# Performance work log

Hardware: AMD Instinct MI355X
Metric: run time of the kernel (lower is better)

The kernel has to match this reference:

```python
import jax, jax.numpy as jnp
import numpy as np

B, S, D, E, K = 4, 4096, 2048, 64, 2

def setup_inputs() -> dict:
    key = jax.random.key(0)
    kx, kw = jax.random.split(key)
    x = jax.random.normal(kx, (B, S, D), dtype=jnp.float32)
    W = jax.random.normal(kw, (E, D), dtype=jnp.float32) * (1.0 / np.sqrt(D))
    b = jnp.zeros((E,), dtype=jnp.float32)
    return {"x": x, "W": W, "b": b, "k": K}

def reference(x, W, b, k):
    # logits: [B, S, E]
    logits = jnp.einsum('bsd,ed->bse', x, W) + b
    probs = jax.nn.softmax(logits, axis=-1)
    topk_probs, topk_experts = jax.lax.top_k(probs, k)  # [B,S,k]
    # one-hot over experts, OR-reduce over k -> bool mask [B,S,E]
    onehot = jax.nn.one_hot(topk_experts, E, dtype=jnp.int32)  # [B,S,k,E]
    masks = onehot.sum(axis=-2).astype(jnp.bool_)
    return (masks, probs)
```

## Files before the change

### kernel.cpp

```cpp
#include <hip/hip_runtime.h>
#include <math.h>

#define NTOK    16384
#define DDIM    2048
#define NEXP    64
#define PSTRIDE (NTOK * NEXP)
#define ITERS   32
#define SLICE_B 8192

#define AS1 __attribute__((address_space(1)))
#define AS3 __attribute__((address_space(3)))

typedef _Float16 half8   __attribute__((ext_vector_type(8)));
typedef float    floatx4 __attribute__((ext_vector_type(4)));

__global__ __launch_bounds__(256) void wconv_kernel(
    const float* __restrict__ W, _Float16* __restrict__ ws)
{
    const int g     = blockIdx.x * 256 + threadIdx.x;
    const int i32   = g >> 9;
    const int L     = g & 511;
    const int plane = L >> 8;
    const int r     = L & 255;
    const int e     = r >> 2;
    const int cp    = r & 3;
    const int c     = cp ^ ((e >> 1) & 3);
    const int k     = (i32 << 5) + (c << 3);

    const float* src = &W[(size_t)e * DDIM + k];
    floatx4 w0 = *(const floatx4*)src;
    floatx4 w1 = *(const floatx4*)(src + 4);

    half8 o;
#pragma unroll
    for (int i = 0; i < 4; ++i) {
        float f0 = w0[i], f1 = w1[i];
        _Float16 h0 = (_Float16)f0, h1 = (_Float16)f1;
        if (plane == 0) { o[i] = h0; o[4 + i] = h1; }
        else {
            o[i]     = (_Float16)((f0 - (float)h0) * 2048.0f);
            o[4 + i] = (_Float16)((f1 - (float)h1) * 2048.0f);
        }
    }
    *(half8*)((char*)ws + (size_t)g * 16) = o;
}

__global__ __launch_bounds__(256, 2) void router_kernel(
    const float* __restrict__ x,
    const _Float16* __restrict__ ws,
    const float* __restrict__ bias,
    float* __restrict__ out)
{
    __shared__ __align__(16) char wlds[4][2][SLICE_B];

    const int tid  = threadIdx.x;
    const int lane = tid & 63;
    const int wid  = tid >> 6;
    const int t    = wid >> 1;
    const int h    = wid & 1;
    const int t0   = blockIdx.x * 32 + t * 16;
    const int mrow = lane & 15;
    const int quad = lane >> 4;

    floatx4 acc_hh[4], acc_md[4];
#pragma unroll
    for (int j = 0; j < 4; ++j) { acc_hh[j] = (floatx4)0.0f; acc_md[j] = (floatx4)0.0f; }

    const float* xrow = x + (size_t)(t0 + mrow) * DDIM + h * 1024 + quad * 8;
    const char* wsrc = (const char*)ws + (size_t)h * 32 * SLICE_B + lane * 16;
    char* buf0 = &wlds[wid][0][0];
    char* buf1 = &wlds[wid][1][0];

    int boff[4];
#pragma unroll
    for (int j = 0; j < 4; ++j) {
        const int e = j * 16 + mrow;
        boff[j] = e * 32 + ((quad ^ ((e >> 1) & 3)) << 3);
    }

#define DMA_SLICE(I, DST)                                                      \
    {                                                                          \
        const char* gs = wsrc + (size_t)(I) * SLICE_B;                         \
        _Pragma("unroll")                                                      \
        for (int q = 0; q < 8; ++q)                                            \
            __builtin_amdgcn_global_load_lds(                                  \
                (const AS1 unsigned int*)(const void*)(gs + q * 1024),         \
                (AS3 unsigned int*)(void*)((DST) + q * 1024), 16, 0, 0);       \
    }

    DMA_SLICE(0, buf0);
    floatx4 xa0 = *(const floatx4*)(xrow);
    floatx4 xa1 = *(const floatx4*)(xrow + 4);
    floatx4 xb0 = *(const floatx4*)(xrow + 32);
    floatx4 xb1 = *(const floatx4*)(xrow + 36);

#pragma unroll 2
    for (int i = 0; i < ITERS; ++i) {
        if (i + 1 < ITERS) DMA_SLICE(i + 1, (i & 1) ? buf0 : buf1);
        floatx4 xn0, xn1;
        if (i + 2 < ITERS) {
            xn0 = *(const floatx4*)(xrow + (i + 2) * 32);
            xn1 = *(const floatx4*)(xrow + (i + 2) * 32 + 4);
        }

        half8 a_hi, a_lo;
#pragma unroll
        for (int q = 0; q < 4; ++q) {
            float fv = xa0[q];
            _Float16 hh = (_Float16)fv;
            a_hi[q] = hh;
            a_lo[q] = (_Float16)((fv - (float)hh) * 2048.0f);
        }
#pragma unroll
        for (int q = 0; q < 4; ++q) {
            float fv = xa1[q];
            _Float16 hh = (_Float16)fv;
            a_hi[4 + q] = hh;
            a_lo[4 + q] = (_Float16)((fv - (float)hh) * 2048.0f);
        }

        const _Float16* lb = (const _Float16*)((i & 1) ? buf1 : buf0);
#pragma unroll
        for (int j = 0; j < 4; ++j) {
            half8 bh = *(const half8*)(lb + boff[j]);
            half8 bl = *(const half8*)(lb + 2048 + boff[j]);
            acc_hh[j] = __builtin_amdgcn_mfma_f32_16x16x32_f16(a_hi, bh, acc_hh[j], 0, 0, 0);
            acc_md[j] = __builtin_amdgcn_mfma_f32_16x16x32_f16(a_hi, bl, acc_md[j], 0, 0, 0);
            acc_md[j] = __builtin_amdgcn_mfma_f32_16x16x32_f16(a_lo, bh, acc_md[j], 0, 0, 0);
        }

        xa0 = xb0; xa1 = xb1; xb0 = xn0; xb1 = xn1;
    }

    float lg[4][4];
#pragma unroll
    for (int j = 0; j < 4; ++j)
#pragma unroll
        for (int r = 0; r < 4; ++r)
            lg[j][r] = acc_hh[j][r] + acc_md[j][r] * (1.0f / 2048.0f);

    __syncthreads();
    float* rbuf = (float*)&wlds[0][0][0];
    if (h == 1) {
#pragma unroll
        for (int j = 0; j < 4; ++j)
#pragma unroll
            for (int r = 0; r < 4; ++r)
                rbuf[t * 1024 + (j * 4 + r) * 64 + lane] = lg[j][r];
    }
    __syncthreads();
    if (h == 1) return;

#pragma unroll
    for (int j = 0; j < 4; ++j) {
        const float bj = bias[j * 16 + mrow];
#pragma unroll
        for (int r = 0; r < 4; ++r)
            lg[j][r] += rbuf[t * 1024 + (j * 4 + r) * 64 + lane] + bj;
    }

    const int c = mrow;
#pragma unroll
    for (int r = 0; r < 4; ++r) {
        const int trow = t0 + quad * 4 + r;

        float m = lg[0][r];
#pragma unroll
        for (int j = 1; j < 4; ++j) m = fmaxf(m, lg[j][r]);
#pragma unroll
        for (int off = 1; off <= 8; off <<= 1) m = fmaxf(m, __shfl_xor(m, off));

        float pj[4], s = 0.0f;
#pragma unroll
        for (int j = 0; j < 4; ++j) { pj[j] = __expf(lg[j][r] - m); s += pj[j]; }
#pragma unroll
        for (int off = 1; off <= 8; off <<= 1) s += __shfl_xor(s, off);
        const float rinv = 1.0f / s;

        float v1 = -1e30f, v2 = -1e30f; int i1 = -1, i2 = -1;
#pragma unroll
        for (int j = 0; j < 4; ++j) {
            float v = lg[j][r]; int e = j * 16 + c;
            if (v > v1 || (v == v1 && e < i1)) { v2 = v1; i2 = i1; v1 = v; i1 = e; }
            else if (v > v2 || (v == v2 && e < i2)) { v2 = v; i2 = e; }
        }
#pragma unroll
        for (int off = 1; off <= 8; off <<= 1) {
            float u1 = __shfl_xor(v1, off); int q1 = __shfl_xor(i1, off);
            float u2 = __shfl_xor(v2, off); int q2 = __shfl_xor(i2, off);
            if (u1 > v1 || (u1 == v1 && q1 < i1)) {
                if (v1 > u2 || (v1 == u2 && i1 < q2)) { v2 = v1; i2 = i1; }
                else                                   { v2 = u2; i2 = q2; }
                v1 = u1; i1 = q1;
            } else {
                if (u1 > v2 || (u1 == v2 && q1 < i2)) { v2 = u1; i2 = q1; }
            }
        }

#pragma unroll
        for (int j = 0; j < 4; ++j) {
            const int col = j * 16 + c;
            const size_t o = (size_t)trow * NEXP + col;
            out[o]           = (col == i1 || col == i2) ? 1.0f : 0.0f;
            out[PSTRIDE + o] = pj[j] * rinv;
        }
    }
}

extern "C" void kernel_launch(void* const* d_in, const int* in_sizes, int n_in,
                              void* d_out, int out_size, void* d_ws, size_t ws_size,
                              hipStream_t stream) {
    const float* x = (const float*)d_in[0];
    const float* W = (const float*)d_in[1];
    const float* b = (const float*)d_in[2];
    (void)in_sizes; (void)n_in; (void)out_size; (void)ws_size;
    float* out = (float*)d_out;

    _Float16* ws = (_Float16*)d_ws;

    hipLaunchKernelGGL(wconv_kernel, dim3(128), dim3(256), 0, stream, W, ws);
    hipLaunchKernelGGL(router_kernel, dim3(NTOK / 32), dim3(256), 0, stream, x, ws, b, out);
}
```

Measured before the change: 225.8 us.

## Load pre-swizzled weight fragments directly from global into registers, drop LDS staging

Reorders the converted fp16 weight workspace so each lane's MFMA B-fragment is a contiguous 16-byte chunk. The router kernel then reads it straight from global/L2 into registers with a one-iteration prefetch, instead of DMAing slices into LDS and reading them back. This removes the LDS staging and the ds_read traffic and shrinks shared memory to the reduction buffer. In exchange, every wave re-reads the weights from cache, and the fully unrolled loop may raise register pressure under the 2-blocks-per-CU launch bound.

Measured after the change: 248.5 us. +10.0%, slower.

```diff
diff --git a/kernel.cpp b/kernel.cpp
--- a/kernel.cpp
+++ b/kernel.cpp
@@ -6,10 +6,6 @@
 #define NEXP    64
 #define PSTRIDE (NTOK * NEXP)
 #define ITERS   32
-#define SLICE_B 8192
-
-#define AS1 __attribute__((address_space(1)))
-#define AS3 __attribute__((address_space(3)))
 
 typedef _Float16 half8   __attribute__((ext_vector_type(8)));
 typedef float    floatx4 __attribute__((ext_vector_type(4)));
@@ -17,15 +13,14 @@
 __global__ __launch_bounds__(256) void wconv_kernel(
     const float* __restrict__ W, _Float16* __restrict__ ws)
 {
-    const int g     = blockIdx.x * 256 + threadIdx.x;
-    const int i32   = g >> 9;
-    const int L     = g & 511;
-    const int plane = L >> 8;
-    const int r     = L & 255;
-    const int e     = r >> 2;
-    const int cp    = r & 3;
-    const int c     = cp ^ ((e >> 1) & 3);
-    const int k     = (i32 << 5) + (c << 3);
+    const int g    = blockIdx.x * 256 + threadIdx.x;
+    const int lane = g & 63;
+    const int pl   = (g >> 6) & 1;
+    const int j    = (g >> 7) & 3;
+    const int i    = (g >> 9) & 31;
+    const int h    = (g >> 14) & 1;
+    const int e    = j * 16 + (lane & 15);
+    const int k    = h * 1024 + i * 32 + (lane >> 4) * 8;
 
     const float* src = &W[(size_t)e * DDIM + k];
     floatx4 w0 = *(const floatx4*)src;
@@ -33,16 +28,16 @@
 
     half8 o;
 #pragma unroll
-    for (int i = 0; i < 4; ++i) {
-        float f0 = w0[i], f1 = w1[i];
+    for (int q = 0; q < 4; ++q) {
+        float f0 = w0[q], f1 = w1[q];
         _Float16 h0 = (_Float16)f0, h1 = (_Float16)f1;
-        if (plane == 0) { o[i] = h0; o[4 + i] = h1; }
+        if (pl == 0) { o[q] = h0; o[4 + q] = h1; }
         else {
-            o[i]     = (_Float16)((f0 - (float)h0) * 2048.0f);
-            o[4 + i] = (_Float16)((f1 - (float)h1) * 2048.0f);
-        }
-    }
-    *(half8*)((char*)ws + (size_t)g * 16) = o;
+            o[q]     = (_Float16)((f0 - (float)h0) * 2048.0f);
+            o[4 + q] = (_Float16)((f1 - (float)h1) * 2048.0f);
+        }
+    }
+    *(half8*)(ws + (size_t)g * 8) = o;
 }
 
 __global__ __launch_bounds__(256, 2) void router_kernel(
@@ -51,7 +46,7 @@
     const float* __restrict__ bias,
     float* __restrict__ out)
 {
-    __shared__ __align__(16) char wlds[4][2][SLICE_B];
+    __shared__ float rbuf[2048];
 
     const int tid  = threadIdx.x;
     const int lane = tid & 63;
@@ -67,69 +62,59 @@
     for (int j = 0; j < 4; ++j) { acc_hh[j] = (floatx4)0.0f; acc_md[j] = (floatx4)0.0f; }
 
     const float* xrow = x + (size_t)(t0 + mrow) * DDIM + h * 1024 + quad * 8;
-    const char* wsrc = (const char*)ws + (size_t)h * 32 * SLICE_B + lane * 16;
-    char* buf0 = &wlds[wid][0][0];
-    char* buf1 = &wlds[wid][1][0];
-
-    int boff[4];
+    const _Float16* wbase = ws + (size_t)h * 131072 + (size_t)lane * 8;
+
+    floatx4 xs0[ITERS], xs1[ITERS];
+    half8   bsh[ITERS][4], bsl[ITERS][4];
+
+#pragma unroll
+    for (int i = 0; i < 2; ++i) {
+        xs0[i] = *(const floatx4*)(xrow + i * 32);
+        xs1[i] = *(const floatx4*)(xrow + i * 32 + 4);
+    }
 #pragma unroll
     for (int j = 0; j < 4; ++j) {
-        const int e = j * 16 + mrow;
-        boff[j] = e * 32 + ((quad ^ ((e >> 1) & 3)) << 3);
-    }
-
-#define DMA_SLICE(I, DST)                                                      \
-    {                                                                          \
-        const char* gs = wsrc + (size_t)(I) * SLICE_B;                         \
-        _Pragma("unroll")                                                      \
-        for (int q = 0; q < 8; ++q)                                            \
-            __builtin_amdgcn_global_load_lds(                                  \
-                (const AS1 unsigned int*)(const void*)(gs + q * 1024),         \
-                (AS3 unsigned int*)(void*)((DST) + q * 1024), 16, 0, 0);       \
-    }
-
-    DMA_SLICE(0, buf0);
-    floatx4 xa0 = *(const floatx4*)(xrow);
-    floatx4 xa1 = *(const floatx4*)(xrow + 4);
-    floatx4 xb0 = *(const floatx4*)(xrow + 32);
-    floatx4 xb1 = *(const floatx4*)(xrow + 36);
-
-#pragma unroll 2
+        bsh[0][j] = *(const half8*)(wbase + (size_t)(j * 2    ) * 512);
+        bsl[0][j] = *(const half8*)(wbase + (size_t)(j * 2 + 1) * 512);
+    }
+
+#pragma unroll
     for (int i = 0; i < ITERS; ++i) {
-        if (i + 1 < ITERS) DMA_SLICE(i + 1, (i & 1) ? buf0 : buf1);
-        floatx4 xn0, xn1;
         if (i + 2 < ITERS) {
-            xn0 = *(const floatx4*)(xrow + (i + 2) * 32);
-            xn1 = *(const floatx4*)(xrow + (i + 2) * 32 + 4);
+            xs0[i + 2] = *(const floatx4*)(xrow + (i + 2) * 32);
+            xs1[i + 2] = *(const floatx4*)(xrow + (i + 2) * 32 + 4);
+        }
+        if (i + 1 < ITERS) {
+            const _Float16* gb = wbase + (size_t)(i + 1) * 4096;
+#pragma unroll
+            for (int j = 0; j < 4; ++j) {
+                bsh[i + 1][j] = *(const half8*)(gb + (size_t)(j * 2    ) * 512);
+                bsl[i + 1][j] = *(const half8*)(gb + (size_t)(j * 2 + 1) * 512);
+            }
         }
 
         half8 a_hi, a_lo;
 #pragma unroll
         for (int q = 0; q < 4; ++q) {
-            float fv = xa0[q];
+            float fv = xs0[i][q];
             _Float16 hh = (_Float16)fv;
             a_hi[q] = hh;
             a_lo[q] = (_Float16)((fv - (float)hh) * 2048.0f);
         }
 #pragma unroll
         for (int q = 0; q < 4; ++q) {
-            float fv = xa1[q];
+            float fv = xs1[i][q];
             _Float16 hh = (_Float16)fv;
             a_hi[4 + q] = hh;
             a_lo[4 + q] = (_Float16)((fv - (float)hh) * 2048.0f);
         }
 
-        const _Float16* lb = (const _Float16*)((i & 1) ? buf1 : buf0);
 #pragma unroll
         for (int j = 0; j < 4; ++j) {
-            half8 bh = *(const half8*)(lb + boff[j]);
-            half8 bl = *(const half8*)(lb + 2048 + boff[j]);
-            acc_hh[j] = __builtin_amdgcn_mfma_f32_16x16x32_f16(a_hi, bh, acc_hh[j], 0, 0, 0);
-            acc_md[j] = __builtin_amdgcn_mfma_f32_16x16x32_f16(a_hi, bl, acc_md[j], 0, 0, 0);
-            acc_md[j] = __builtin_amdgcn_mfma_f32_16x16x32_f16(a_lo, bh, acc_md[j], 0, 0, 0);
-        }
-
-        xa0 = xb0; xa1 = xb1; xb0 = xn0; xb1 = xn1;
+            acc_hh[j] = __builtin_amdgcn_mfma_f32_16x16x32_f16(a_hi, bsh[i][j], acc_hh[j], 0, 0, 0);
+            acc_md[j] = __builtin_amdgcn_mfma_f32_16x16x32_f16(a_hi, bsl[i][j], acc_md[j], 0, 0, 0);
+            acc_md[j] = __builtin_amdgcn_mfma_f32_16x16x32_f16(a_lo, bsh[i][j], acc_md[j], 0, 0, 0);
+        }
     }
 
     float lg[4][4];
@@ -140,7 +125,6 @@
             lg[j][r] = acc_hh[j][r] + acc_md[j][r] * (1.0f / 2048.0f);
 
     __syncthreads();
-    float* rbuf = (float*)&wlds[0][0][0];
     if (h == 1) {
 #pragma unroll
         for (int j = 0; j < 4; ++j)
```

## Share weight LDS slices across waves with 4-way K split per block

Applied to the files above, without the earlier changes.

Each block now runs 512 threads (8 waves: 2 token tiles × 4 K-quarters), and a single double-buffered 32KB LDS slice per phase is loaded cooperatively and shared by all waves. Before, each wave staged its own private weight copy. The weight workspace layout and swizzle are changed to match, and partial logits from three K-quarters are reduced through LDS. This cuts redundant LDS weight traffic per block and raises the wave count. In exchange it adds a block-wide __syncthreads on every phase and a larger cross-wave reduction.

After: 204.6 us. 1.1x faster.

```diff
diff --git a/kernel.cpp b/kernel.cpp
--- a/kernel.cpp
+++ b/kernel.cpp
@@ -5,8 +5,8 @@
 #define DDIM    2048
 #define NEXP    64
 #define PSTRIDE (NTOK * NEXP)
-#define ITERS   32
-#define SLICE_B 8192
+#define NPH     16
+#define SLICE_B 32768
 
 #define AS1 __attribute__((address_space(1)))
 #define AS3 __attribute__((address_space(3)))
@@ -17,15 +17,15 @@
 __global__ __launch_bounds__(256) void wconv_kernel(
     const float* __restrict__ W, _Float16* __restrict__ ws)
 {
-    const int g     = blockIdx.x * 256 + threadIdx.x;
-    const int i32   = g >> 9;
-    const int L     = g & 511;
-    const int plane = L >> 8;
-    const int r     = L & 255;
-    const int e     = r >> 2;
-    const int cp    = r & 3;
-    const int c     = cp ^ ((e >> 1) & 3);
-    const int k     = (i32 << 5) + (c << 3);
+    const int g  = blockIdx.x * 256 + threadIdx.x;
+    const int p  = g >> 11;
+    const int L  = g & 2047;
+    const int qp = L & 3;
+    const int e  = (L >> 2) & 63;
+    const int pl = (L >> 8) & 1;
+    const int h  = (L >> 9) & 3;
+    const int q  = qp ^ ((e ^ (e >> 2)) & 3);
+    const int k  = h * 512 + p * 32 + q * 8;
 
     const float* src = &W[(size_t)e * DDIM + k];
     floatx4 w0 = *(const floatx4*)src;
@@ -36,28 +36,28 @@
     for (int i = 0; i < 4; ++i) {
         float f0 = w0[i], f1 = w1[i];
         _Float16 h0 = (_Float16)f0, h1 = (_Float16)f1;
-        if (plane == 0) { o[i] = h0; o[4 + i] = h1; }
+        if (pl == 0) { o[i] = h0; o[4 + i] = h1; }
         else {
             o[i]     = (_Float16)((f0 - (float)h0) * 2048.0f);
             o[4 + i] = (_Float16)((f1 - (float)h1) * 2048.0f);
         }
     }
-    *(half8*)((char*)ws + (size_t)g * 16) = o;
+    *(half8*)(ws + (size_t)g * 8) = o;
 }
 
-__global__ __launch_bounds__(256, 2) void router_kernel(
+__global__ __launch_bounds__(512, 4) void router_kernel(
     const float* __restrict__ x,
     const _Float16* __restrict__ ws,
     const float* __restrict__ bias,
     float* __restrict__ out)
 {
-    __shared__ __align__(16) char wlds[4][2][SLICE_B];
+    __shared__ __align__(16) char lds[2][SLICE_B];
 
     const int tid  = threadIdx.x;
     const int lane = tid & 63;
     const int wid  = tid >> 6;
-    const int t    = wid >> 1;
-    const int h    = wid & 1;
+    const int t    = wid >> 2;
+    const int h    = wid & 3;
     const int t0   = blockIdx.x * 32 + t * 16;
     const int mrow = lane & 15;
     const int quad = lane >> 4;
@@ -66,70 +66,69 @@
 #pragma unroll
     for (int j = 0; j < 4; ++j) { acc_hh[j] = (floatx4)0.0f; acc_md[j] = (floatx4)0.0f; }
 
-    const float* xrow = x + (size_t)(t0 + mrow) * DDIM + h * 1024 + quad * 8;
-    const char* wsrc = (const char*)ws + (size_t)h * 32 * SLICE_B + lane * 16;
-    char* buf0 = &wlds[wid][0][0];
-    char* buf1 = &wlds[wid][1][0];
+    const float* xrow = x + (size_t)(t0 + mrow) * DDIM + h * 512 + quad * 8;
 
     int boff[4];
 #pragma unroll
     for (int j = 0; j < 4; ++j) {
         const int e = j * 16 + mrow;
-        boff[j] = e * 32 + ((quad ^ ((e >> 1) & 3)) << 3);
-    }
-
-#define DMA_SLICE(I, DST)                                                      \
+        const int s = (e ^ (e >> 2)) & 3;
+        boff[j] = (((h * 2) * 64 + e) * 4 + (quad ^ s)) * 8;
+    }
+
+#define DMA(P, B)                                                              \
     {                                                                          \
-        const char* gs = wsrc + (size_t)(I) * SLICE_B;                         \
+        const char* gs = (const char*)ws + (size_t)(P) * SLICE_B + (size_t)tid * 16; \
+        char*       ld = &lds[B][0] + tid * 16;                                \
         _Pragma("unroll")                                                      \
-        for (int q = 0; q < 8; ++q)                                            \
+        for (int i_ = 0; i_ < 4; ++i_)                                         \
             __builtin_amdgcn_global_load_lds(                                  \
-                (const AS1 unsigned int*)(const void*)(gs + q * 1024),         \
-                (AS3 unsigned int*)(void*)((DST) + q * 1024), 16, 0, 0);       \
-    }
-
-    DMA_SLICE(0, buf0);
-    floatx4 xa0 = *(const floatx4*)(xrow);
-    floatx4 xa1 = *(const floatx4*)(xrow + 4);
-    floatx4 xb0 = *(const floatx4*)(xrow + 32);
-    floatx4 xb1 = *(const floatx4*)(xrow + 36);
+                (const AS1 unsigned int*)(const void*)(gs + i_ * 8192),        \
+                (AS3 unsigned int*)(void*)(ld + i_ * 8192), 16, 0, 0);         \
+    }
+
+    DMA(0, 0);
+    floatx4 xc0 = *(const floatx4*)(xrow);
+    floatx4 xc1 = *(const floatx4*)(xrow + 4);
+    __syncthreads();
 
 #pragma unroll 2
-    for (int i = 0; i < ITERS; ++i) {
-        if (i + 1 < ITERS) DMA_SLICE(i + 1, (i & 1) ? buf0 : buf1);
+    for (int p = 0; p < NPH; ++p) {
         floatx4 xn0, xn1;
-        if (i + 2 < ITERS) {
-            xn0 = *(const floatx4*)(xrow + (i + 2) * 32);
-            xn1 = *(const floatx4*)(xrow + (i + 2) * 32 + 4);
+        if (p < NPH - 1) {
+            DMA(p + 1, (p + 1) & 1);
+            xn0 = *(const floatx4*)(xrow + (p + 1) * 32);
+            xn1 = *(const floatx4*)(xrow + (p + 1) * 32 + 4);
         }
 
         half8 a_hi, a_lo;
 #pragma unroll
         for (int q = 0; q < 4; ++q) {
-            float fv = xa0[q];
+            float fv = xc0[q];
             _Float16 hh = (_Float16)fv;
             a_hi[q] = hh;
             a_lo[q] = (_Float16)((fv - (float)hh) * 2048.0f);
         }
 #pragma unroll
         for (int q = 0; q < 4; ++q) {
-            float fv = xa1[q];
+            float fv = xc1[q];
             _Float16 hh = (_Float16)fv;
             a_hi[4 + q] = hh;
             a_lo[4 + q] = (_Float16)((fv - (float)hh) * 2048.0f);
         }
 
-        const _Float16* lb = (const _Float16*)((i & 1) ? buf1 : buf0);
+        const _Float16* lb = (const _Float16*)lds[p & 1];
 #pragma unroll
         for (int j = 0; j < 4; ++j) {
             half8 bh = *(const half8*)(lb + boff[j]);
-            half8 bl = *(const half8*)(lb + 2048 + boff[j]);
+            half8 bl = *(const half8*)(lb + boff[j] + 2048);
             acc_hh[j] = __builtin_amdgcn_mfma_f32_16x16x32_f16(a_hi, bh, acc_hh[j], 0, 0, 0);
             acc_md[j] = __builtin_amdgcn_mfma_f32_16x16x32_f16(a_hi, bl, acc_md[j], 0, 0, 0);
             acc_md[j] = __builtin_amdgcn_mfma_f32_16x16x32_f16(a_lo, bh, acc_md[j], 0, 0, 0);
         }
 
-        xa0 = xb0; xa1 = xb1; xb0 = xn0; xb1 = xn1;
+        if (p < NPH - 1) { xc0 = xn0; xc1 = xn1; }
+        __syncthreads();
     }
 
     float lg[4][4];
@@ -139,24 +138,26 @@
         for (int r = 0; r < 4; ++r)
             lg[j][r] = acc_hh[j][r] + acc_md[j][r] * (1.0f / 2048.0f);
 
+    float* rbuf = (float*)&lds[0][0];
+    if (h > 0) {
+#pragma unroll
+        for (int j = 0; j < 4; ++j)
+#pragma unroll
+            for (int r = 0; r < 4; ++r)
+                rbuf[((h - 1) * 2 + t) * 1024 + (j * 4 + r) * 64 + lane] = lg[j][r];
+    }
     __syncthreads();
-    float* rbuf = (float*)&wlds[0][0][0];
-    if (h == 1) {
-#pragma unroll
-        for (int j = 0; j < 4; ++j)
-#pragma unroll
-            for (int r = 0; r < 4; ++r)
-                rbuf[t * 1024 + (j * 4 + r) * 64 + lane] = lg[j][r];
-    }
-    __syncthreads();
-    if (h == 1) return;
+    if (h > 0) return;
 
 #pragma unroll
     for (int j = 0; j < 4; ++j) {
         const float bj = bias[j * 16 + mrow];
 #pragma unroll
-        for (int r = 0; r < 4; ++r)
-            lg[j][r] += rbuf[t * 1024 + (j * 4 + r) * 64 + lane] + bj;
+        for (int r = 0; r < 4; ++r) {
+            const int f = (j * 4 + r) * 64 + lane;
+            lg[j][r] += rbuf[t * 1024 + f] + rbuf[(2 + t) * 1024 + f]
+                      + rbuf[(4 + t) * 1024 + f] + bj;
+        }
     }
 
     const int c = mrow;
@@ -218,6 +219,6 @@
 
     _Float16* ws = (_Float16*)d_ws;
 
-    hipLaunchKernelGGL(wconv_kernel, dim3(128), dim3(256), 0, stream, W, ws);
-    hipLaunchKernelGGL(router_kernel, dim3(NTOK / 32), dim3(256), 0, stream, x, ws, b, out);
+    hipLaunchKernelGGL(wconv_kernel,  dim3(128), dim3(256), 0, stream, W, ws);
+    hipLaunchKernelGGL(router_kernel, dim3(NTOK / 32), dim3(512), 0, stream, x, ws, b, out);
 }
```
